# Kernel optimization log

Hardware: AMD Instinct MI355X
Metric: run time of the kernel (lower is better)

The kernel has to match this reference:

```python
import jax, jax.numpy as jnp
import numpy as np

B, L, CIN, COUT, TEMB, N_MODES = 32, 8192, 64, 64, 256, 64
M = N_MODES // 2 + 1  # retained rfft modes = 33
EPS = 1e-5


def setup_inputs() -> dict:
    key = jax.random.key(0)
    ks = jax.random.split(key, 12)
    std_w = float(np.sqrt(1.0 / (2.0 * CIN)))
    # flax Dense default kernel init = lecun_normal ~ normal(std=1/sqrt(fan_in)); plain normal is fine for a reference
    return {
        "x": jax.random.normal(ks[0], (B, L, CIN), jnp.float32),
        "t_emb": jax.random.normal(ks[1], (B, TEMB), jnp.float32),
        # SpectralFreqTimeConv1D params
        "spec_w_real": jax.random.normal(ks[2], (M, CIN, COUT), jnp.float32) * std_w,
        "spec_w_imag": jax.random.normal(ks[3], (M, CIN, COUT), jnp.float32) * std_w,
        "dense_re": jax.random.normal(ks[4], (TEMB, M), jnp.float32) / np.sqrt(TEMB),
        "dense_im": jax.random.normal(ks[5], (TEMB, M), jnp.float32) / np.sqrt(TEMB),
        # TimeConv1D params
        "conv_kernel": jax.random.normal(ks[6], (CIN, COUT), jnp.float32) / np.sqrt(CIN),
        "conv_bias": jnp.zeros((COUT,), jnp.float32),
        "tc_weights": jax.random.normal(ks[7], (COUT, COUT), jnp.float32) * 0.01,  # nn.initializers.normal() stddev=0.01
        "psi_kernel": jax.random.normal(ks[8], (TEMB, 2 * COUT), jnp.float32) / np.sqrt(TEMB),
        # BatchNorm params
        "bn_scale": jnp.ones((COUT,), jnp.float32),
        "bn_bias": jnp.zeros((COUT,), jnp.float32),
    }


def reference(x, t_emb, spec_w_real, spec_w_imag, dense_re, dense_im,
              conv_kernel, conv_bias, tc_weights, psi_kernel, bn_scale, bn_bias):
    b, L_in, _ = x.shape
    n_freq = L_in // 2 + 1

    # ---- SpectralFreqTimeConv1D ----
    x_ft = jnp.fft.rfft(x, axis=-2, norm="forward")            # (b, n_freq, CIN) complex
    t_c = (t_emb @ dense_re) + 1j * (t_emb @ dense_im)         # (b, M) complex
    W = spec_w_real + 1j * spec_w_imag                          # (M, CIN, COUT) complex
    # diagonal-in-mode modulation: equivalent to the eye-based einsum chain
    out_m = t_c[:, :, None] * jnp.einsum("bmi,mio->bmo", x_ft[:, :M, :], W)  # (b, M, COUT)
    out_ft = jnp.zeros((b, n_freq, COUT), jnp.complex64).at[:, :M, :].set(out_m)
    x_spec = jnp.fft.irfft(out_ft, axis=-2, n=L_in, norm="forward")  # (b, L, COUT)

    # ---- TimeConv1D (residual branch) ----
    h = x @ conv_kernel + conv_bias                             # 1x1 conv: (b, L, COUT)
    psi = t_emb @ psi_kernel                                    # (b, 2*COUT)
    w_t, b_t = jnp.split(psi, 2, axis=-1)
    # einsum('ij,bjk,blk->bli', W, diag(w_t), h) == (h * w_t) @ W^T
    x_res = jnp.einsum("blj,ij->bli", h * w_t[:, None, :], tc_weights) + b_t[:, None, :]

    # ---- combine, batchnorm (training: batch stats), activation ----
    out = x_spec + x_res
    mean = out.mean(axis=(0, 1))
    var = out.var(axis=(0, 1))
    out = (out - mean) * jax.lax.rsqrt(var + EPS) * bn_scale + bn_bias
    return jax.nn.relu(out)
```

## Files before the change

### kernel.cpp

```cpp
#include <hip/hip_runtime.h>

typedef short short8 __attribute__((ext_vector_type(8)));
typedef float f32x4 __attribute__((ext_vector_type(4)));
typedef unsigned int u32;
typedef u32 u32x4 __attribute__((ext_vector_type(4)));
typedef unsigned short u16;

#define BB 32
#define LL 8192
#define TE 256
#define MM 33
#define INVL (1.0f/8192.0f)
#define TWOPI 6.28318530717958647692f

#define TBLM_OFF 0
#define TTD_OFF  262144
#define VTB_OFF  589824
#define DD_OFF   720896
#define DD2_OFF  722944
#define BNP_OFF  731200

#define PART_OFF  0
#define SRED2_OFF 9437184
#define VF_OFF    9732096

static __device__ __forceinline__ u16 f2b(float f) {
  u32 u = __float_as_uint(f);
  return (u16)((u + 0x7FFFu + ((u >> 16) & 1u)) >> 16);
}
static __device__ __forceinline__ u32 pk2(float lo, float hi) {
  return __builtin_amdgcn_perm(__float_as_uint(hi) + 0x8000u,
                               __float_as_uint(lo) + 0x8000u,
                               0x07060302u);
}

static __device__ __forceinline__ float slot_val(int j, int l) {
  int m = (j == 0) ? 32 : (j <= 32 ? j : j - 32);
  bool is_sin = (j == 0) || (j >= 33);
  int r = (m * l) & (LL - 1);
  float ang = (float)r * (TWOPI / (float)LL);
  return is_sin ? sinf(ang) : cosf(ang);
}

__global__ __launch_bounds__(256) void k_tbl(float* __restrict__ ws) {
  int bid = blockIdx.x;
  if (bid < 2048) {
    int idx = bid * 256 + threadIdx.x;
    int l = idx >> 6, j = idx & 63;
    ((u16*)ws)[TBLM_OFF * 2 + idx] = f2b(slot_val(j, l));
  } else {
    int bb = bid - 2048;
    int j = bb >> 5;
    int l = (bb & 31) * 256 + threadIdx.x;
    float v = (j < 64) ? slot_val(j, l) : (j == 64 ? 1.0f : 0.0f);
    ((u16*)ws)[TTD_OFF * 2 + j * LL + l] = f2b(v);
  }
}

__global__ __launch_bounds__(576) void k_dft(const float* __restrict__ x,
                                             const float* __restrict__ ws,
                                             float* __restrict__ scr) {
  __shared__ __align__(16) u16 sX[2][64 * 136];
  int tid = threadIdx.x;
  int b = blockIdx.x >> 5, chunk = blockIdx.x & 31;
  int l0 = chunk * 256;
  int w = tid >> 6, lane = tid & 63;
  const u16* tt = (const u16*)ws + TTD_OFF * 2;

  f32x4 acc[4];
#pragma unroll
  for (int ct = 0; ct < 4; ++ct) acc[ct] = (f32x4){0.f, 0.f, 0.f, 0.f};

  int arow = lane & 15;
  int kb = (lane >> 4) * 8;
  bool isg = (w >= 5);
  int gi = w - 5;
  bool stg = (tid < 512);
  int sc = tid & 63, lg = (tid >> 6) & 7;

  float vx[16];
  if (stg) {
#pragma unroll
    for (int i = 0; i < 16; ++i)
      vx[i] = x[(b * LL + l0 + lg * 16 + i) * 64 + sc];
    u32 wv[8];
#pragma unroll
    for (int j = 0; j < 8; ++j) wv[j] = pk2(vx[2 * j], vx[2 * j + 1]);
    u32x4* dst = (u32x4*)&sX[0][sc * 136 + lg * 16];
    dst[0] = (u32x4){wv[0], wv[1], wv[2], wv[3]};
    dst[1] = (u32x4){wv[4], wv[5], wv[6], wv[7]};
  }
  __syncthreads();

  if (stg) {
#pragma unroll
    for (int i = 0; i < 16; ++i)
      vx[i] = x[(b * LL + l0 + 128 + lg * 16 + i) * 64 + sc];
  }

#pragma unroll
  for (int kk = 0; kk < 4; ++kk) {
    short8 a = isg
      ? *reinterpret_cast<const short8*>(&sX[0][(gi * 16 + arow) * 136 + kk * 32 + kb])
      : *reinterpret_cast<const short8*>(tt + (w * 16 + arow) * LL + l0 + kk * 32 + kb);
#pragma unroll
    for (int ct = 0; ct < 4; ++ct) {
      short8 bf = *reinterpret_cast<const short8*>(&sX[0][(ct * 16 + arow) * 136 + kk * 32 + kb]);
      acc[ct] = __builtin_amdgcn_mfma_f32_16x16x32_bf16(a, bf, acc[ct], 0, 0, 0);
    }
  }

  if (stg) {
    u32 wv[8];
#pragma unroll
    for (int j = 0; j < 8; ++j) wv[j] = pk2(vx[2 * j], vx[2 * j + 1]);
    u32x4* dst = (u32x4*)&sX[1][sc * 136 + lg * 16];
    dst[0] = (u32x4){wv[0], wv[1], wv[2], wv[3]};
    dst[1] = (u32x4){wv[4], wv[5], wv[6], wv[7]};
  }
  __syncthreads();

#pragma unroll
  for (int kk = 0; kk < 4; ++kk) {
    short8 a = isg
      ? *reinterpret_cast<const short8*>(&sX[1][(gi * 16 + arow) * 136 + kk * 32 + kb])
      : *reinterpret_cast<const short8*>(tt + (w * 16 + arow) * LL + l0 + 128 + kk * 32 + kb);
#pragma unroll
    for (int ct = 0; ct < 4; ++ct) {
      short8 bf = *reinterpret_cast<const short8*>(&sX[1][(ct * 16 + arow) * 136 + kk * 32 + kb]);
      acc[ct] = __builtin_amdgcn_mfma_f32_16x16x32_bf16(a, bf, acc[ct], 0, 0, 0);
    }
  }

  int rowbase = isg ? (80 + gi * 16) : (w * 16);
  int rowb = (lane >> 4) * 4;
#pragma unroll
  for (int ct = 0; ct < 4; ++ct) {
    int col = ct * 16 + (lane & 15);
#pragma unroll
    for (int r = 0; r < 4; ++r)
      scr[PART_OFF + ((b * 32 + chunk) * 144 + rowbase + rowb + r) * 64 + col] = acc[ct][r];
  }
}

__global__ __launch_bounds__(256) void k_red1(float* __restrict__ scr) {
  int b = blockIdx.y;
  int r = blockIdx.x * 256 + threadIdx.x;
  float a = 0.f;
#pragma unroll 8
  for (int ch = 0; ch < 32; ++ch) a += scr[PART_OFF + (b * 32 + ch) * 9216 + r];
  scr[SRED2_OFF + b * 9216 + r] = a;
}

__global__ __launch_bounds__(256) void k_vb(
    const float* __restrict__ t_emb, const float* __restrict__ dre,
    const float* __restrict__ dim_, const float* __restrict__ pk,
    const float* __restrict__ swr, const float* __restrict__ swi,
    const float* __restrict__ ck, const float* __restrict__ cbias,
    const float* __restrict__ tw, float* __restrict__ scr,
    float* __restrict__ ws) {
  __shared__ float smem[12352];
  int tid = threadIdx.x;

  if (blockIdx.x < 33) {
    int m = blockIdx.x;
    float2* sW = (float2*)smem;
    float2* sX = (float2*)(smem + 8192);
    float* sTcb = smem + 8192 + 4096;

    for (int idx = tid; idx < 8192; idx += 256) smem[idx] = t_emb[idx];
    __syncthreads();
    if (tid < 64) {
      int b = tid & 31;
      const float* dd = (tid < 32) ? dre : dim_;
      float a = 0.f;
#pragma unroll 8
      for (int j = 0; j < TE; ++j) a = fmaf(smem[b * 256 + j], dd[j * MM + m], a);
      sTcb[tid] = a;
    }
    __syncthreads();

    for (int idx = tid; idx < 4096; idx += 256)
      sW[idx] = make_float2(swr[m * 4096 + idx], swi[m * 4096 + idx]);
    for (int idx = tid; idx < 2048; idx += 256) {
      int b = idx >> 6, i = idx & 63;
      const float* sr = scr + SRED2_OFF + b * 9216;
      float xr, xi;
      if (m == 0)      { xr = sr[64 * 64 + i] * INVL;  xi = 0.f; }
      else if (m < 32) { xr = sr[m * 64 + i] * INVL;   xi = -sr[(32 + m) * 64 + i] * INVL; }
      else             { xr = sr[32 * 64 + i] * INVL;  xi = -sr[0 * 64 + i] * INVL; }
      sX[idx] = make_float2(xr, xi);
    }
    __syncthreads();

    int w = tid >> 6, lane = tid & 63;
    for (int p = 0; p < 8; ++p) {
      int b = p * 4 + w;
      float a0 = 0.f, a1 = 0.f, a2 = 0.f, a3 = 0.f;
#pragma unroll 16
      for (int i = 0; i < 64; ++i) {
        float2 wv = sW[i * 64 + lane];
        float2 xv = sX[b * 64 + i];
        a0 = fmaf(xv.x, wv.x, a0);
        a1 = fmaf(xv.y, wv.y, a1);
        a2 = fmaf(xv.x, wv.y, a2);
        a3 = fmaf(xv.y, wv.x, a3);
      }
      float ar = a0 - a1, ai = a2 + a3;
      float tcr = sTcb[b], tci = sTcb[32 + b];
      float cr = tcr * ar - tci * ai;
      float ci = tcr * ai + tci * ar;
      if (m == 0) {
        ws[DD2_OFF + b * 64 + lane] = cr;
      } else {
        float crr = 2.f * cr, cii = -2.f * ci;
        int js = (m == 32) ? 0 : 32 + m;
        u16* vtb = (u16*)ws + VTB_OFF * 2 + (b * 64 + lane) * 128;
        vtb[64 + m] = f2b(crr);
        vtb[64 + js] = f2b(cii);
        float* vf = scr + VF_OFF + b * 8192;
        vf[(64 + m) * 64 + lane] = crr;
        vf[(64 + js) * 64 + lane] = cii;
      }
    }
  } else {
    int b = blockIdx.x - 33;
    float* sCkT = smem;
    float* sPtw = smem + 4096;
    float* sTe  = smem + 8192;
    float* sPsi = smem + 8448;

    sTe[tid] = t_emb[b * 256 + tid];
    __syncthreads();
    if (tid < 128) {
      float a = 0.f;
#pragma unroll 8
      for (int j = 0; j < TE; ++j) a = fmaf(sTe[j], pk[j * 128 + tid], a);
      sPsi[tid] = a;
    }
    __syncthreads();
    for (int idx = tid; idx < 4096; idx += 256) {
      int c = idx >> 6, j = idx & 63;
      sCkT[j * 64 + c] = ck[idx];
      sPtw[idx] = sPsi[j] * tw[idx];
    }
    __syncthreads();

    u16* vtb = (u16*)ws + VTB_OFF * 2 + b * 64 * 128;
    float* vf = scr + VF_OFF + b * 8192;
    int lane = tid & 63, w = tid >> 6;
#pragma unroll 4
    for (int it = 0; it < 16; ++it) {
      int o = it * 4 + w;
      float a = 0.f;
#pragma unroll 16
      for (int j = 0; j < 64; ++j)
        a = fmaf(sCkT[j * 64 + lane], sPtw[o * 64 + j], a);
      vtb[o * 128 + lane] = f2b(a);
      vf[lane * 64 + o] = a;
    }
    if (tid < 64) {
      float a = 0.f;
      for (int j = 0; j < 64; ++j) a = fmaf(cbias[j], sPtw[tid * 64 + j], a);
      ws[DD_OFF + b * 64 + tid] = a + sPsi[64 + tid];
    }
  }
}

__global__ __launch_bounds__(256) void k_bn(const float* __restrict__ scr,
                                            float* __restrict__ ws) {
  __shared__ float sVx[64 * 64];
  __shared__ float sGx[64 * 64];
  __shared__ float sS[64 * 64];
  __shared__ float sSum[64];
  __shared__ float sP[4][2][64];
  int tid = threadIdx.x, b = blockIdx.x;
  const float* sr = scr + SRED2_OFF + b * 9216;
  const float* vf = scr + VF_OFF + b * 8192;

  for (int p = tid; p < 4096; p += 256) {
    sVx[p] = vf[p];
    sGx[p] = sr[80 * 64 + p];
    sS[p]  = sr[p];
  }
  if (tid < 64) sSum[tid] = sr[64 * 64 + tid];
  __syncthreads();

  int o = tid & 63, part = tid >> 6;
  float m1 = 0.f, q1 = 0.f, cross = 0.f, vt2 = 0.f;
  for (int ii = 0; ii < 16; ++ii) {
    int i = part * 16 + ii;
    float vx = sVx[i * 64 + o];
    m1 = fmaf(sSum[i], vx, m1);
    float w0 = 0.f, w1 = 0.f, c0 = 0.f, c1 = 0.f;
#pragma unroll
    for (int j = 0; j < 64; j += 2) {
      float va = sVx[j * 64 + o], vb = sVx[(j + 1) * 64 + o];
      w0 = fmaf(sGx[i * 64 + j], va, w0);
      w1 = fmaf(sGx[i * 64 + j + 1], vb, w1);
      c0 = fmaf(sS[i * 64 + j], va, c0);
      c1 = fmaf(sS[i * 64 + j + 1], vb, c1);
    }
    q1 = fmaf(vx, w0 + w1, q1);
    float vt = vf[(64 + i) * 64 + o];
    vt2 = fmaf(vt, vt, vt2);
    cross = fmaf(vt, c0 + c1, cross);
  }
  sP[part][0][o] = m1;
  sP[part][1][o] = q1 + 2.f * cross + 4096.f * vt2;
  __syncthreads();
  if (tid < 64) {
    float m = sP[0][0][tid] + sP[1][0][tid] + sP[2][0][tid] + sP[3][0][tid];
    float q = sP[0][1][tid] + sP[1][1][tid] + sP[2][1][tid] + sP[3][1][tid];
    float D = ws[DD_OFF + b * 64 + tid] + ws[DD2_OFF + b * 64 + tid];
    ws[BNP_OFF + b * 128 + tid]      = m + 8192.f * D;
    ws[BNP_OFF + b * 128 + 64 + tid] = q + 2.f * D * m + 8192.f * D * D;
  }
}

__global__ __launch_bounds__(256) void k_main(const float* __restrict__ x,
                                              const float* __restrict__ ws,
                                              const float* __restrict__ bns,
                                              const float* __restrict__ bnb,
                                              float* __restrict__ out) {
  __shared__ __align__(16) u16 sVt[64 * 136];
  __shared__ float sD[64];
  __shared__ float sA[64];
  __shared__ float sB[64];
  __shared__ float sPp[4][64];
  __shared__ float sPq[4][64];
  int tid = threadIdx.x, w = tid >> 6, lane = tid & 63;
  int b = blockIdx.x >> 6, rg = blockIdx.x & 63;
  const u16* wsu = (const u16*)ws;

  {
    const u32* src = (const u32*)(wsu + VTB_OFF * 2 + b * 64 * 128);
    u32* dst = (u32*)sVt;
    for (int p = tid; p < 4096; p += 256)
      dst[(p >> 6) * 68 + (p & 63)] = src[p];
  }
  {
    int o = tid & 63, g = tid >> 6;
    float pm = 0.f, pq = 0.f;
#pragma unroll
    for (int r = 0; r < 8; ++r) {
      int bb = g * 8 + r;
      pm += ws[BNP_OFF + bb * 128 + o];
      pq += ws[BNP_OFF + bb * 128 + 64 + o];
    }
    sPp[g][o] = pm;
    sPq[g][o] = pq;
  }
  if (tid < 64) sD[tid] = ws[DD_OFF + b * 64 + tid] + ws[DD2_OFF + b * 64 + tid];
  __syncthreads();
  if (tid < 64) {
    const float inv_n = 1.f / (32.f * 8192.f);
    float mean = (sPp[0][tid] + sPp[1][tid] + sPp[2][tid] + sPp[3][tid]) * inv_n;
    float ex2  = (sPq[0][tid] + sPq[1][tid] + sPq[2][tid] + sPq[3][tid]) * inv_n;
    float var = ex2 - mean * mean;
    float istd = rsqrtf(var + 1e-5f);
    float al = istd * bns[tid];
    sA[tid] = al;
    sB[tid] = bnb[tid] - mean * al;
  }
  __syncthreads();

  int kb = (lane >> 4) * 8;
  short8 bf[4][4];
#pragma unroll
  for (int kk = 0; kk < 4; ++kk)
#pragma unroll
    for (int ct = 0; ct < 4; ++ct)
      bf[kk][ct] = *reinterpret_cast<const short8*>(
          &sVt[(ct * 16 + (lane & 15)) * 136 + kk * 32 + kb]);

  const u16* tb = wsu + TBLM_OFF * 2;
  int rowb = (lane >> 4) * 4;
  int lbase = rg * 128 + w * 32;

#pragma unroll
  for (int rt = 0; rt < 2; ++rt) {
    int l = lbase + rt * 16 + (lane & 15);
    const float* xq = x + (b * LL + l) * 64;
    float4 u0 = *reinterpret_cast<const float4*>(xq + kb);
    float4 u1 = *reinterpret_cast<const float4*>(xq + kb + 4);
    float4 u2 = *reinterpret_cast<const float4*>(xq + 32 + kb);
    float4 u3 = *reinterpret_cast<const float4*>(xq + 32 + kb + 4);
    union { short8 s; u32 wv[4]; } A0, A1;
    A0.wv[0] = pk2(u0.x, u0.y); A0.wv[1] = pk2(u0.z, u0.w);
    A0.wv[2] = pk2(u1.x, u1.y); A0.wv[3] = pk2(u1.z, u1.w);
    A1.wv[0] = pk2(u2.x, u2.y); A1.wv[1] = pk2(u2.z, u2.w);
    A1.wv[2] = pk2(u3.x, u3.y); A1.wv[3] = pk2(u3.z, u3.w);
    short8 a2 = *reinterpret_cast<const short8*>(tb + l * 64 + kb);
    short8 a3 = *reinterpret_cast<const short8*>(tb + l * 64 + 32 + kb);

    f32x4 acc[4];
#pragma unroll
    for (int ct = 0; ct < 4; ++ct) acc[ct] = (f32x4){0.f, 0.f, 0.f, 0.f};
#pragma unroll
    for (int ct = 0; ct < 4; ++ct) {
      acc[ct] = __builtin_amdgcn_mfma_f32_16x16x32_bf16(A0.s, bf[0][ct], acc[ct], 0, 0, 0);
      acc[ct] = __builtin_amdgcn_mfma_f32_16x16x32_bf16(A1.s, bf[1][ct], acc[ct], 0, 0, 0);
      acc[ct] = __builtin_amdgcn_mfma_f32_16x16x32_bf16(a2, bf[2][ct], acc[ct], 0, 0, 0);
      acc[ct] = __builtin_amdgcn_mfma_f32_16x16x32_bf16(a3, bf[3][ct], acc[ct], 0, 0, 0);
    }
#pragma unroll
    for (int ct = 0; ct < 4; ++ct) {
      int o = ct * 16 + (lane & 15);
      float dd = sD[o], al = sA[o], be = sB[o];
#pragma unroll
      for (int r = 0; r < 4; ++r) {
        float v = acc[ct][r] + dd;
        out[(b * LL + lbase + rt * 16 + rowb + r) * 64 + o] =
            fmaxf(fmaf(v, al, be), 0.f);
      }
    }
  }
}

extern "C" void kernel_launch(void* const* d_in, const int* in_sizes, int n_in,
                              void* d_out, int out_size, void* d_ws, size_t ws_size,
                              hipStream_t stream) {
  const float* x     = (const float*)d_in[0];
  const float* t_emb = (const float*)d_in[1];
  const float* swr   = (const float*)d_in[2];
  const float* swi   = (const float*)d_in[3];
  const float* dre   = (const float*)d_in[4];
  const float* dim_  = (const float*)d_in[5];
  const float* ck    = (const float*)d_in[6];
  const float* cbias = (const float*)d_in[7];
  const float* tw    = (const float*)d_in[8];
  const float* pk    = (const float*)d_in[9];
  const float* bns   = (const float*)d_in[10];
  const float* bnb   = (const float*)d_in[11];
  float* ws  = (float*)d_ws;
  float* out = (float*)d_out;

  k_tbl<<<4608, 256, 0, stream>>>(ws);
  k_dft<<<1024, 576, 0, stream>>>(x, ws, out);
  k_red1<<<dim3(36, 32), 256, 0, stream>>>(out);
  k_vb<<<65, 256, 0, stream>>>(t_emb, dre, dim_, pk, swr, swi,
                               ck, cbias, tw, out, ws);
  k_bn<<<32, 256, 0, stream>>>(out, ws);
  k_main<<<2048, 256, 0, stream>>>(x, ws, bns, bnb, out);
}
```

Measured before the change: 101.4 us.

## Fold chunk reduction into consumers and use hardware sin/cos for tables

Removes the separate k_red1 reduction kernel: k_vb and k_bn now sum the 32 per-chunk DFT partials directly when loading their shared inputs. This saves one launch and the write and re-read of the reduced buffer, but the reads are now done by only 65 and 32 blocks. The twiddle-table kernel switches to v_sin/v_cos intrinsics taking revolutions, computes each cos/sin pair in one thread, and writes the constant rows with a plain store, using fewer blocks. The hardware sin/cos are less accurate than sinf/cosf, though the results are rounded to bf16 anyway.

```diff
diff --git a/kernel.cpp b/kernel.cpp
--- a/kernel.cpp
+++ b/kernel.cpp
@@ -11,7 +11,6 @@
 #define TE 256
 #define MM 33
 #define INVL (1.0f/8192.0f)
-#define TWOPI 6.28318530717958647692f
 
 #define TBLM_OFF 0
 #define TTD_OFF  262144
@@ -21,7 +20,6 @@
 #define BNP_OFF  731200
 
 #define PART_OFF  0
-#define SRED2_OFF 9437184
 #define VF_OFF    9732096
 
 static __device__ __forceinline__ u16 f2b(float f) {
@@ -33,27 +31,36 @@
                                __float_as_uint(lo) + 0x8000u,
                                0x07060302u);
 }
-
-static __device__ __forceinline__ float slot_val(int j, int l) {
-  int m = (j == 0) ? 32 : (j <= 32 ? j : j - 32);
-  bool is_sin = (j == 0) || (j >= 33);
-  int r = (m * l) & (LL - 1);
-  float ang = (float)r * (TWOPI / (float)LL);
-  return is_sin ? sinf(ang) : cosf(ang);
-}
+static __device__ __forceinline__ float fsin(float rev) {
+  float r; asm("v_sin_f32 %0, %1" : "=v"(r) : "v"(rev)); return r;
+}
+static __device__ __forceinline__ float fcos(float rev) {
+  float r; asm("v_cos_f32 %0, %1" : "=v"(r) : "v"(rev)); return r;
+}
+
 
 __global__ __launch_bounds__(256) void k_tbl(float* __restrict__ ws) {
-  int bid = blockIdx.x;
-  if (bid < 2048) {
-    int idx = bid * 256 + threadIdx.x;
-    int l = idx >> 6, j = idx & 63;
-    ((u16*)ws)[TBLM_OFF * 2 + idx] = f2b(slot_val(j, l));
+  u16* tb = (u16*)ws;
+  u16* tt = (u16*)ws + TTD_OFF * 2;
+  int bid = blockIdx.x, tid = threadIdx.x;
+  if (bid < 1024) {
+    int t = bid * 256 + tid;
+    int l = t >> 5, m = (t & 31) + 1;
+    float rev = (float)((m * l) & (LL - 1)) * INVL;
+    int js = (m == 32) ? 0 : 32 + m;
+    tb[l * 64 + m]  = f2b(fcos(rev));
+    tb[l * 64 + js] = f2b(fsin(rev));
+  } else if (bid < 2048) {
+    int t = (bid - 1024) * 256 + tid;
+    int m = (t >> 13) + 1, l = t & (LL - 1);
+    float rev = (float)((m * l) & (LL - 1)) * INVL;
+    int js = (m == 32) ? 0 : 32 + m;
+    tt[m * LL + l]  = f2b(fcos(rev));
+    tt[js * LL + l] = f2b(fsin(rev));
   } else {
-    int bb = bid - 2048;
-    int j = bb >> 5;
-    int l = (bb & 31) * 256 + threadIdx.x;
-    float v = (j < 64) ? slot_val(j, l) : (j == 64 ? 1.0f : 0.0f);
-    ((u16*)ws)[TTD_OFF * 2 + j * LL + l] = f2b(v);
+    int t = (bid - 2048) * 256 + tid;
+    int r = t >> 13;
+    tt[(64 + r) * LL + (t & (LL - 1))] = (r == 0) ? 0x3F80u : 0u;
   }
 }
 
@@ -143,15 +150,6 @@
   }
 }
 
-__global__ __launch_bounds__(256) void k_red1(float* __restrict__ scr) {
-  int b = blockIdx.y;
-  int r = blockIdx.x * 256 + threadIdx.x;
-  float a = 0.f;
-#pragma unroll 8
-  for (int ch = 0; ch < 32; ++ch) a += scr[PART_OFF + (b * 32 + ch) * 9216 + r];
-  scr[SRED2_OFF + b * 9216 + r] = a;
-}
-
 __global__ __launch_bounds__(256) void k_vb(
     const float* __restrict__ t_emb, const float* __restrict__ dre,
     const float* __restrict__ dim_, const float* __restrict__ pk,
@@ -184,12 +182,25 @@
       sW[idx] = make_float2(swr[m * 4096 + idx], swi[m * 4096 + idx]);
     for (int idx = tid; idx < 2048; idx += 256) {
       int b = idx >> 6, i = idx & 63;
-      const float* sr = scr + SRED2_OFF + b * 9216;
-      float xr, xi;
-      if (m == 0)      { xr = sr[64 * 64 + i] * INVL;  xi = 0.f; }
-      else if (m < 32) { xr = sr[m * 64 + i] * INVL;   xi = -sr[(32 + m) * 64 + i] * INVL; }
-      else             { xr = sr[32 * 64 + i] * INVL;  xi = -sr[0 * 64 + i] * INVL; }
-      sX[idx] = make_float2(xr, xi);
+      const float* pb = scr + PART_OFF + b * 32 * 9216;
+      float xr = 0.f, xi = 0.f;
+      if (m == 0) {
+#pragma unroll 8
+        for (int ch = 0; ch < 32; ++ch) xr += pb[ch * 9216 + 64 * 64 + i];
+      } else if (m < 32) {
+#pragma unroll 8
+        for (int ch = 0; ch < 32; ++ch) {
+          xr += pb[ch * 9216 + m * 64 + i];
+          xi -= pb[ch * 9216 + (32 + m) * 64 + i];
+        }
+      } else {
+#pragma unroll 8
+        for (int ch = 0; ch < 32; ++ch) {
+          xr += pb[ch * 9216 + 32 * 64 + i];
+          xi -= pb[ch * 9216 + i];
+        }
+      }
+      sX[idx] = make_float2(xr * INVL, xi * INVL);
     }
     __syncthreads();
 
@@ -275,15 +286,26 @@
   __shared__ float sSum[64];
   __shared__ float sP[4][2][64];
   int tid = threadIdx.x, b = blockIdx.x;
-  const float* sr = scr + SRED2_OFF + b * 9216;
+  const float* pb = scr + PART_OFF + b * 32 * 9216;
   const float* vf = scr + VF_OFF + b * 8192;
 
   for (int p = tid; p < 4096; p += 256) {
+    float gx = 0.f, ss = 0.f;
+#pragma unroll 8
+    for (int ch = 0; ch < 32; ++ch) {
+      gx += pb[ch * 9216 + 80 * 64 + p];
+      ss += pb[ch * 9216 + p];
+    }
+    sGx[p] = gx;
+    sS[p] = ss;
     sVx[p] = vf[p];
-    sGx[p] = sr[80 * 64 + p];
-    sS[p]  = sr[p];
-  }
-  if (tid < 64) sSum[tid] = sr[64 * 64 + tid];
+  }
+  if (tid < 64) {
+    float a = 0.f;
+#pragma unroll 8
+    for (int ch = 0; ch < 32; ++ch) a += pb[ch * 9216 + 64 * 64 + tid];
+    sSum[tid] = a;
+  }
   __syncthreads();
 
   int o = tid & 63, part = tid >> 6;
@@ -374,7 +396,7 @@
       bf[kk][ct] = *reinterpret_cast<const short8*>(
           &sVt[(ct * 16 + (lane & 15)) * 136 + kk * 32 + kb]);
 
-  const u16* tb = wsu + TBLM_OFF * 2;
+  const u16* tb = wsu;
   int rowb = (lane >> 4) * 4;
   int lbase = rg * 128 + w * 32;
 
@@ -436,9 +458,8 @@
   float* ws  = (float*)d_ws;
   float* out = (float*)d_out;
 
-  k_tbl<<<4608, 256, 0, stream>>>(ws);
+  k_tbl<<<2560, 256, 0, stream>>>(ws);
   k_dft<<<1024, 576, 0, stream>>>(x, ws, out);
-  k_red1<<<dim3(36, 32), 256, 0, stream>>>(out);
   k_vb<<<65, 256, 0, stream>>>(t_emb, dre, dim_, pk, swr, swi,
                                ck, cbias, tw, out, ws);
   k_bn<<<32, 256, 0, stream>>>(out, ws);
```

Result: slower. 176.6 us (+74.1%).
